# Kernel optimization log

Measured on AMD Instinct MI355X. Metric: run time of the kernel, lower is better.

The kernel has to match this reference:

```python
import jax, jax.numpy as jnp
import numpy as np

NUM_MODES = 256
IN_FEATURES = 256
OUT_FEATURES = 64
LAYERS = 256   # brick-wall mesh depth
PAIRS = 128    # disjoint adjacent-mode pairs per layer
BATCH = 131072


def setup_inputs() -> dict:
    key = jax.random.key(0)
    kx, kt, kp, ko = jax.random.split(key, 4)
    x = jax.random.normal(kx, (BATCH, IN_FEATURES), dtype=jnp.float32)
    theta = jax.random.uniform(kt, (LAYERS, PAIRS), dtype=jnp.float32, minval=0.0, maxval=float(np.pi))
    phi = jax.random.uniform(kp, (LAYERS, PAIRS), dtype=jnp.float32, minval=0.0, maxval=float(2 * np.pi))
    output_phases = jax.random.uniform(ko, (NUM_MODES,), dtype=jnp.float32, minval=0.0, maxval=float(2 * np.pi))
    # Clements-style brick-wall layout: even layers pair (0,1),(2,3),...;
    # odd layers pair (1,2),(3,4),... with a periodic wrap pair (255,0).
    m1 = np.zeros((LAYERS, PAIRS), np.int32)
    m2 = np.zeros((LAYERS, PAIRS), np.int32)
    for l in range(LAYERS):
        idx = (l % 2 + 2 * np.arange(PAIRS)) % NUM_MODES
        m1[l] = idx
        m2[l] = (idx + 1) % NUM_MODES
    return {
        "x": x,
        "theta": theta,
        "phi": phi,
        "output_phases": output_phases,
        "mode1": jnp.asarray(m1),
        "mode2": jnp.asarray(m2),
    }


def _normalize_optical_params(theta, phi):
    # theta -> [0, pi/2], phi -> [0, 2pi), mirroring normalize_optical_params
    theta = theta % np.pi
    flip = theta > (np.pi / 2)
    theta = jnp.where(flip, np.pi - theta, theta)
    phi = jnp.where(flip, phi + np.pi, phi) % (2.0 * np.pi)
    return theta, phi


def _build_transformation(theta, phi, output_phases, mode1, mode2):
    """Compose the interferometer unitary U = D(out_phases) * T_K * ... * T_1,
    where each T_k is a beamsplitter Givens rotation:
      T[m1,m1]=e^{i phi} cos(t), T[m1,m2]=-sin(t),
      T[m2,m1]=e^{i phi} sin(t), T[m2,m2]= cos(t).
    Pairs within one layer are disjoint, so a whole layer is applied at once."""
    theta, phi = _normalize_optical_params(theta, phi)
    U0 = jnp.eye(NUM_MODES, dtype=jnp.complex64)

    def layer(U, inputs):
        m1, m2, th, ph = inputs              # each [PAIRS]
        r1, r2 = U[m1], U[m2]                # [PAIRS, NUM_MODES]
        e = jnp.exp(1j * ph)[:, None]        # complex64 [PAIRS, 1]
        c = jnp.cos(th)[:, None]
        s = jnp.sin(th)[:, None]
        U = U.at[m1].set(e * c * r1 - s * r2)
        U = U.at[m2].set(e * s * r1 + c * r2)
        return U, None

    U, _ = jax.lax.scan(layer, U0, (mode1, mode2, theta, phi))
    U = jnp.exp(1j * output_phases)[:, None] * U
    return jnp.real(U).astype(jnp.float32)   # [NUM_MODES, NUM_MODES]


def reference(x, theta, phi, output_phases, mode1, mode2):
    T = _build_transformation(theta, phi, output_phases, mode1, mode2)
    # input mask is all-ones (in_features == num_modes); output mask keeps the
    # first OUT_FEATURES modes, then output is sliced to OUT_FEATURES, which
    # is equivalent to using the first OUT_FEATURES rows of T directly.
    T_eff = T[:OUT_FEATURES]                 # [OUT_FEATURES, NUM_MODES]
    return x @ T_eff.T                       # [BATCH, OUT_FEATURES]
```

## Files before the change

### kernel.cpp

```cpp
#include <hip/hip_runtime.h>
#include <hip/hip_bf16.h>
#include <cstdint>
#include <cstddef>

#define PI_F 3.14159265358979323846f
#define TWO_PI_F 6.28318530717958647692f

typedef __bf16 bf16x8 __attribute__((ext_vector_type(8)));
typedef __bf16 bf16x4 __attribute__((ext_vector_type(4)));
typedef float  f32x4  __attribute__((ext_vector_type(4)));

__device__ __forceinline__ __bf16 to_bf16(float f) { return (__bf16)f; }

__global__ __launch_bounds__(256) void olk_params(
    const float* __restrict__ theta, const float* __restrict__ phi,
    float4* __restrict__ t4, float2* __restrict__ t2) {
  int idx = blockIdx.x * 256 + threadIdx.x;
  float t = fmodf(theta[idx], PI_F);
  float p = phi[idx];
  if (t > 0.5f * PI_F) { t = PI_F - t; p += PI_F; }
  p = fmodf(p, TWO_PI_F);
  float c  = cosf(t), s  = sinf(t);
  float cp = cosf(p), sp = sinf(p);
  t4[idx] = make_float4(cp * c, sp * c, cp * s, sp * s);
  t2[idx] = make_float2(c, s);
}

struct P8 {
  float4 qa[8];
  float4 qb[8];
  float4 cc[8];
};

template<bool TBL>
__device__ __forceinline__ void loadP8(P8& P, int lb, int lane,
    const float4* __restrict__ t4, const float2* __restrict__ t2,
    const float* __restrict__ theta, const float* __restrict__ phi) {
  if (TBL) {
#pragma unroll
    for (int k = 0; k < 8; ++k) {
      int idx = (lb + k) * 128 + 2 * lane;
      P.qa[k] = t4[idx];
      P.qb[k] = t4[idx + 1];
      P.cc[k] = *(const float4*)&t2[idx];
    }
  } else {
#pragma unroll
    for (int k = 0; k < 8; ++k) {
      int idx = (lb + k) * 128 + 2 * lane;
      float2 th = *(const float2*)&theta[idx];
      float2 ph = *(const float2*)&phi[idx];
      float ta = fmodf(th.x, PI_F), pa = ph.x;
      if (ta > 0.5f * PI_F) { ta = PI_F - ta; pa += PI_F; }
      pa = fmodf(pa, TWO_PI_F);
      float tb = fmodf(th.y, PI_F), pb = ph.y;
      if (tb > 0.5f * PI_F) { tb = PI_F - tb; pb += PI_F; }
      pb = fmodf(pb, TWO_PI_F);
      float ca = cosf(ta), sa = sinf(ta), cpa = cosf(pa), spa = sinf(pa);
      float cb = cosf(tb), sb = sinf(tb), cpb = cosf(pb), spb = sinf(pb);
      P.qa[k] = make_float4(cpa * ca, spa * ca, cpa * sa, spa * sa);
      P.qb[k] = make_float4(cpb * cb, spb * cb, cpb * sb, spb * sb);
      P.cc[k] = make_float4(ca, sa, cb, sb);
    }
  }
}

__device__ __forceinline__ void layer_step(bool odd, int lane,
    float4 qa, float4 qb, float4 cc,
    float& vre0, float& vim0, float& vre1, float& vim1,
    float& vre2, float& vim2, float& vre3, float& vim3) {
  if (!odd) {
    float nr0 = qa.x * vre0 - qa.y * vim0 + qa.z * vre1 - qa.w * vim1;
    float ni0 = qa.x * vim0 + qa.y * vre0 + qa.z * vim1 + qa.w * vre1;
    float nr1 = cc.x * vre1 - cc.y * vre0;
    float ni1 = cc.x * vim1 - cc.y * vim0;
    float nr2 = qb.x * vre2 - qb.y * vim2 + qb.z * vre3 - qb.w * vim3;
    float ni2 = qb.x * vim2 + qb.y * vre2 + qb.z * vim3 + qb.w * vre3;
    float nr3 = cc.z * vre3 - cc.w * vre2;
    float ni3 = cc.z * vim3 - cc.w * vim2;
    vre0 = nr0; vim0 = ni0; vre1 = nr1; vim1 = ni1;
    vre2 = nr2; vim2 = ni2; vre3 = nr3; vim3 = ni3;
  } else {
    int nxt = (lane + 1) & 63, prv = (lane + 63) & 63;
    float xre = __shfl(vre0, nxt, 64);
    float xim = __shfl(vim0, nxt, 64);
    float pre = __shfl(vre3, prv, 64);
    float pim = __shfl(vim3, prv, 64);
    float cp  = __shfl(cc.z, prv, 64);
    float sp  = __shfl(cc.w, prv, 64);
    float nr1 = qa.x * vre1 - qa.y * vim1 + qa.z * vre2 - qa.w * vim2;
    float ni1 = qa.x * vim1 + qa.y * vre1 + qa.z * vim2 + qa.w * vre2;
    float nr2 = cc.x * vre2 - cc.y * vre1;
    float ni2 = cc.x * vim2 - cc.y * vim1;
    float nr3 = qb.x * vre3 - qb.y * vim3 + qb.z * xre - qb.w * xim;
    float ni3 = qb.x * vim3 + qb.y * vre3 + qb.z * xim + qb.w * xre;
    float nr0 = cp * vre0 - sp * pre;
    float ni0 = cp * vim0 - sp * pim;
    vre0 = nr0; vim0 = ni0; vre1 = nr1; vim1 = ni1;
    vre2 = nr2; vim2 = ni2; vre3 = nr3; vim3 = ni3;
  }
}

template<bool TBL>
__global__ __launch_bounds__(256) void olk_build(
    const float* __restrict__ theta, const float* __restrict__ phi,
    const float* __restrict__ outph,
    const float4* __restrict__ t4, const float2* __restrict__ t2,
    __bf16* __restrict__ Tb) {
  int lane = threadIdx.x & 63;
  int r = blockIdx.x * 4 + (threadIdx.x >> 6);
  int c0 = lane * 4;
  float vre0 = (c0 + 0 == r) ? 1.f : 0.f, vim0 = 0.f;
  float vre1 = (c0 + 1 == r) ? 1.f : 0.f, vim1 = 0.f;
  float vre2 = (c0 + 2 == r) ? 1.f : 0.f, vim2 = 0.f;
  float vre3 = (c0 + 3 == r) ? 1.f : 0.f, vim3 = 0.f;

  P8 A, B;
  loadP8<TBL>(A, 31 * 8, lane, t4, t2, theta, phi);
  for (int it = 0; it < 16; ++it) {
    int bA = 31 - 2 * it;
    int bB = bA - 1;
    loadP8<TBL>(B, bB * 8, lane, t4, t2, theta, phi);
#pragma unroll
    for (int k = 7; k >= 0; --k)
      layer_step((k & 1) != 0, lane, A.qa[k], A.qb[k], A.cc[k],
                 vre0, vim0, vre1, vim1, vre2, vim2, vre3, vim3);
    if (it < 15)
      loadP8<TBL>(A, (bB - 1) * 8, lane, t4, t2, theta, phi);
#pragma unroll
    for (int k = 7; k >= 0; --k)
      layer_step((k & 1) != 0, lane, B.qa[k], B.qb[k], B.cc[k],
                 vre0, vim0, vre1, vim1, vre2, vim2, vre3, vim3);
  }

  float oph = outph[r];
  float co = cosf(oph), so = sinf(oph);
  bf16x4 o;
  o[0] = to_bf16(co * vre0 - so * vim0);
  o[1] = to_bf16(co * vre1 - so * vim1);
  o[2] = to_bf16(co * vre2 - so * vim2);
  o[3] = to_bf16(co * vre3 - so * vim3);
  *(bf16x4*)(Tb + r * 256 + c0) = o;
}

union FragB { bf16x8 v; uint2 u2[2]; };
union FragA { bf16x8 v; };

__global__ __launch_bounds__(256, 2) void olk_mm(
    const float* __restrict__ x, const __bf16* __restrict__ Tb,
    float* __restrict__ out) {
  int lane = threadIdx.x & 63;
  int gw = blockIdx.x * 4 + (threadIdx.x >> 6);
  int l15 = lane & 15, lg = lane >> 4;

  FragB b[4][8];
#pragma unroll
  for (int nt = 0; nt < 4; ++nt) {
#pragma unroll
    for (int ks = 0; ks < 8; ++ks) {
      int row = nt * 16 + l15;
      int col = ks * 32 + 4 * lg;
      b[nt][ks].u2[0] = *(const uint2*)(Tb + row * 256 + col);
      b[nt][ks].u2[1] = *(const uint2*)(Tb + row * 256 + col + 16);
    }
  }

#pragma unroll 1
  for (int t = 0; t < 4; ++t) {
    int mt = gw * 4 + t;
    const float* xr = x + (size_t)(mt * 16 + l15) * 256 + 4 * lg;

    f32x4 acc[4];
#pragma unroll
    for (int nt = 0; nt < 4; ++nt) acc[nt] = (f32x4){0.f, 0.f, 0.f, 0.f};

    FragA a[8];
#pragma unroll
    for (int ks = 0; ks < 8; ++ks) {
      float4 lo = *(const float4*)(xr + ks * 32);
      float4 hi = *(const float4*)(xr + ks * 32 + 16);
      a[ks].v[0] = to_bf16(lo.x); a[ks].v[1] = to_bf16(lo.y);
      a[ks].v[2] = to_bf16(lo.z); a[ks].v[3] = to_bf16(lo.w);
      a[ks].v[4] = to_bf16(hi.x); a[ks].v[5] = to_bf16(hi.y);
      a[ks].v[6] = to_bf16(hi.z); a[ks].v[7] = to_bf16(hi.w);
    }

#pragma unroll
    for (int ks = 0; ks < 8; ++ks) {
#pragma unroll
      for (int nt = 0; nt < 4; ++nt)
        acc[nt] = __builtin_amdgcn_mfma_f32_16x16x32_bf16(
            a[ks].v, b[nt][ks].v, acc[nt], 0, 0, 0);
    }

    float* ob = out + (size_t)(mt * 16) * 64;
#pragma unroll
    for (int r = 0; r < 4; ++r) {
      int row = 4 * lg + r;
#pragma unroll
      for (int nt = 0; nt < 4; ++nt)
        ob[row * 64 + nt * 16 + l15] = acc[nt][r];
    }
  }
}

extern "C" void kernel_launch(void* const* d_in, const int* in_sizes, int n_in,
                              void* d_out, int out_size, void* d_ws, size_t ws_size,
                              hipStream_t stream) {
  const float* x     = (const float*)d_in[0];
  const float* theta = (const float*)d_in[1];
  const float* phi   = (const float*)d_in[2];
  const float* outph = (const float*)d_in[3];
  float* out = (float*)d_out;

  char* ws = (char*)d_ws;
  bool tbl = ws_size >= (size_t)(832 * 1024);
  float4* t4 = (float4*)ws;
  float2* t2 = (float2*)(ws + 512 * 1024);
  __bf16* Tb = (__bf16*)(ws + (tbl ? 768 * 1024 : 0));

  if (tbl) {
    olk_params<<<128, 256, 0, stream>>>(theta, phi, t4, t2);
    olk_build<true><<<16, 256, 0, stream>>>(theta, phi, outph, t4, t2, Tb);
  } else {
    olk_build<false><<<16, 256, 0, stream>>>(theta, phi, outph, nullptr, nullptr, Tb);
  }
  olk_mm<<<512, 256, 0, stream>>>(x, Tb, out);
}
```

Before: 92.69 us.

## Split GEMM output columns across waves and raise occupancy in olk_mm

Each wave now owns one 16-column slice of the output and keeps only 8 B fragments, while the four waves in a block share the same row tiles. The grid doubles and launch bounds allow four blocks per CU, reducing register pressure to improve latency hiding. In exchange, every wave reloads and converts the same x rows, quadrupling fp32-to-bf16 conversion and relying on caches to absorb the repeated global reads.

```diff
diff --git a/kernel.cpp b/kernel.cpp
--- a/kernel.cpp
+++ b/kernel.cpp
@@ -146,61 +146,50 @@
 union FragB { bf16x8 v; uint2 u2[2]; };
 union FragA { bf16x8 v; };
 
-__global__ __launch_bounds__(256, 2) void olk_mm(
+__global__ __launch_bounds__(256, 4) void olk_mm(
     const float* __restrict__ x, const __bf16* __restrict__ Tb,
     float* __restrict__ out) {
   int lane = threadIdx.x & 63;
-  int gw = blockIdx.x * 4 + (threadIdx.x >> 6);
+  int w = threadIdx.x >> 6;
   int l15 = lane & 15, lg = lane >> 4;
 
-  FragB b[4][8];
-#pragma unroll
-  for (int nt = 0; nt < 4; ++nt) {
+  FragB b[8];
+#pragma unroll
+  for (int ks = 0; ks < 8; ++ks) {
+    int row = w * 16 + l15;
+    int col = ks * 32 + 4 * lg;
+    b[ks].u2[0] = *(const uint2*)(Tb + row * 256 + col);
+    b[ks].u2[1] = *(const uint2*)(Tb + row * 256 + col + 16);
+  }
+
+#pragma unroll 1
+  for (int t = 0; t < 8; ++t) {
+    int mt = blockIdx.x * 8 + t;
+    const float* xr = x + (size_t)(mt * 16 + l15) * 256 + 4 * lg;
+
+    f32x4 acc = (f32x4){0.f, 0.f, 0.f, 0.f};
+
+    float4 lo[8], hi[8];
 #pragma unroll
     for (int ks = 0; ks < 8; ++ks) {
-      int row = nt * 16 + l15;
-      int col = ks * 32 + 4 * lg;
-      b[nt][ks].u2[0] = *(const uint2*)(Tb + row * 256 + col);
-      b[nt][ks].u2[1] = *(const uint2*)(Tb + row * 256 + col + 16);
-    }
-  }
-
-#pragma unroll 1
-  for (int t = 0; t < 4; ++t) {
-    int mt = gw * 4 + t;
-    const float* xr = x + (size_t)(mt * 16 + l15) * 256 + 4 * lg;
-
-    f32x4 acc[4];
-#pragma unroll
-    for (int nt = 0; nt < 4; ++nt) acc[nt] = (f32x4){0.f, 0.f, 0.f, 0.f};
-
-    FragA a[8];
+      lo[ks] = *(const float4*)(xr + ks * 32);
+      hi[ks] = *(const float4*)(xr + ks * 32 + 16);
+    }
+
 #pragma unroll
     for (int ks = 0; ks < 8; ++ks) {
-      float4 lo = *(const float4*)(xr + ks * 32);
-      float4 hi = *(const float4*)(xr + ks * 32 + 16);
-      a[ks].v[0] = to_bf16(lo.x); a[ks].v[1] = to_bf16(lo.y);
-      a[ks].v[2] = to_bf16(lo.z); a[ks].v[3] = to_bf16(lo.w);
-      a[ks].v[4] = to_bf16(hi.x); a[ks].v[5] = to_bf16(hi.y);
-      a[ks].v[6] = to_bf16(hi.z); a[ks].v[7] = to_bf16(hi.w);
-    }
-
-#pragma unroll
-    for (int ks = 0; ks < 8; ++ks) {
-#pragma unroll
-      for (int nt = 0; nt < 4; ++nt)
-        acc[nt] = __builtin_amdgcn_mfma_f32_16x16x32_bf16(
-            a[ks].v, b[nt][ks].v, acc[nt], 0, 0, 0);
-    }
-
-    float* ob = out + (size_t)(mt * 16) * 64;
-#pragma unroll
-    for (int r = 0; r < 4; ++r) {
-      int row = 4 * lg + r;
-#pragma unroll
-      for (int nt = 0; nt < 4; ++nt)
-        ob[row * 64 + nt * 16 + l15] = acc[nt][r];
-    }
+      FragA a;
+      a.v[0] = to_bf16(lo[ks].x); a.v[1] = to_bf16(lo[ks].y);
+      a.v[2] = to_bf16(lo[ks].z); a.v[3] = to_bf16(lo[ks].w);
+      a.v[4] = to_bf16(hi[ks].x); a.v[5] = to_bf16(hi[ks].y);
+      a.v[6] = to_bf16(hi[ks].z); a.v[7] = to_bf16(hi[ks].w);
+      acc = __builtin_amdgcn_mfma_f32_16x16x32_bf16(a.v, b[ks].v, acc, 0, 0, 0);
+    }
+
+    float* ob = out + (size_t)(mt * 16) * 64 + w * 16 + l15;
+#pragma unroll
+    for (int r = 0; r < 4; ++r)
+      ob[(4 * lg + r) * 64] = acc[r];
   }
 }
 
@@ -225,5 +214,5 @@
   } else {
     olk_build<false><<<16, 256, 0, stream>>>(theta, phi, outph, nullptr, nullptr, Tb);
   }
-  olk_mm<<<512, 256, 0, stream>>>(x, Tb, out);
-}
+  olk_mm<<<1024, 256, 0, stream>>>(x, Tb, out);
+}
```

Result: slower. 120.3 us (+29.8%).
